# Kernel optimization log

Hardware: AMD Instinct MI355X
Metric: run time of the kernel (lower is better)

The kernel has to match this reference:

```python
import jax, jax.numpy as jnp
import numpy as np

B, N, K, F, L, H, ZMAX = 16, 1024, 16, 128, 4, 128, 100


def setup_inputs() -> dict:
    key = jax.random.key(0)
    ks = jax.random.split(key, 12)
    cell = jnp.eye(3, dtype=jnp.float32)[None] * 8.0 + 0.05 * jax.random.normal(ks[0], (B, 3, 3), dtype=jnp.float32)
    x = jax.random.uniform(ks[1], (B, N, 3), dtype=jnp.float32)
    z = jax.random.randint(ks[2], (B, N), 0, ZMAX)
    struct_size = jnp.full((B,), N, dtype=jnp.int32)
    emb = 0.02 * jax.random.normal(ks[3], (ZMAX, F), dtype=jnp.float32)
    din = 2 * F + 1
    W1 = jax.random.normal(ks[4], (L, din, F), dtype=jnp.float32) / np.sqrt(din)
    b1 = jnp.zeros((L, F), dtype=jnp.float32)
    W2 = jax.random.normal(ks[5], (L, F, F), dtype=jnp.float32) / np.sqrt(F)
    b2 = jnp.zeros((L, F), dtype=jnp.float32)
    A1 = jax.random.normal(ks[6], (din, H), dtype=jnp.float32) / np.sqrt(din)
    a1 = jnp.zeros((H,), dtype=jnp.float32)
    A2 = jax.random.normal(ks[7], (H, 1), dtype=jnp.float32) / np.sqrt(H)
    a2 = jnp.zeros((1,), dtype=jnp.float32)
    return {"cell": cell, "x": x, "z": z, "struct_size": struct_size, "emb": emb,
            "W1": W1, "b1": b1, "W2": W2, "b2": b2, "A1": A1, "a1": a1, "A2": A2, "a2": a2}


def _periodic_knn(cell, frac, k):
    # frac: [B,N,3] fractional coords, cell: [B,3,3] lattice rows.
    b, n, _ = frac.shape
    g = jnp.arange(-1, 2, dtype=frac.dtype)
    shifts = jnp.stack(jnp.meshgrid(g, g, g, indexing="ij"), -1).reshape(-1, 3)  # [27,3]
    rel = frac[:, None, :, :] - frac[:, :, None, :]  # rel[b,i,j] = frac_j - frac_i, [B,N,N,3]

    def body(carry, si):
        bd2, bsi = carry
        s, i = si
        cart = jnp.einsum("bijd,bde->bije", rel + s, cell)
        d2 = jnp.sum(cart * cart, axis=-1)
        upd = d2 < bd2
        return (jnp.where(upd, d2, bd2), jnp.where(upd, i, bsi)), None

    init = (jnp.full((b, n, n), 1e30, dtype=frac.dtype), jnp.zeros((b, n, n), dtype=jnp.int32))
    (d2min, simin), _ = jax.lax.scan(body, init, (shifts, jnp.arange(27, dtype=jnp.int32)))
    eye = jnp.eye(n, dtype=bool)
    d2min = jnp.where(eye[None], 1e30, d2min)  # exclude self (zero-shift) edges
    _, idx = jax.lax.top_k(-d2min, k)  # [B,N,k] neighbor indices
    sid = jnp.take_along_axis(simin, idx, axis=2)  # best image shift per edge
    svec = shifts[sid]  # [B,N,k,3]
    frac_j = jax.vmap(lambda f, i: f[i])(frac, idx)  # [B,N,k,3]
    vec = jnp.einsum("bnkd,bde->bnke", frac_j - frac[:, :, None, :] + svec, cell)
    d = jnp.sqrt(jnp.maximum(jnp.sum(vec * vec, axis=-1), 1e-12))  # [B,N,k]
    return idx, vec, d


def _edge_feat(h, idx, d):
    hj = jax.vmap(lambda hb, ib: hb[ib])(h, idx)  # [B,N,k,F]
    hi = jnp.broadcast_to(h[:, :, None, :], hj.shape)
    return jnp.concatenate([hi, hj, d[..., None]], axis=-1)  # [B,N,k,2F+1]


def reference(cell, x, z, struct_size, emb, W1, b1, W2, b2, A1, a1, A2, a2):
    frac = jnp.mod(x, 1.0)
    idx, vec, d = _periodic_knn(cell, frac, K)
    h = emb[z]  # [B,N,F]
    for l in range(W1.shape[0]):
        feat = _edge_feat(h, idx, d)
        m = jax.nn.silu(feat @ W1[l] + b1[l]) @ W2[l] + b2[l]  # [B,N,k,F]
        h = h + jnp.mean(m, axis=2)
    feat = _edge_feat(h, idx, d)
    w = jax.nn.silu(feat @ A1 + a1) @ A2 + a2  # [B,N,k,1]
    delta_cart = jnp.sum(w * vec, axis=2)  # [B,N,3]
    delta_frac = jnp.einsum("bnd,bde->bne", delta_cart, jnp.linalg.inv(cell))
    return x + delta_frac
```

## Files before the change

### kernel.cpp

```cpp
#include <hip/hip_runtime.h>

#define B_ 16
#define N_ 1024
#define K_ 16
#define F_ 128
#define L_ 4
#define DIN_ 257

typedef __bf16 bf16x8 __attribute__((ext_vector_type(8)));
typedef float f32x4 __attribute__((ext_vector_type(4)));

__device__ __forceinline__ float silu_f(float x) {
    return x / (1.0f + __expf(-x));
}

__device__ __forceinline__ unsigned short f2bf_bits(float f) {
    unsigned u = __builtin_bit_cast(unsigned, f);
    return (unsigned short)((u + 0x7FFFu + ((u >> 16) & 1u)) >> 16);
}

__global__ __launch_bounds__(256) void k_prep(const int* __restrict__ z,
                                              const float* __restrict__ emb,
                                              const float* __restrict__ W1,
                                              const float* __restrict__ W2,
                                              const float* __restrict__ A1,
                                              float* __restrict__ h,
                                              unsigned short* __restrict__ hbf,
                                              unsigned short* __restrict__ Wt1,
                                              unsigned short* __restrict__ Wt2,
                                              unsigned short* __restrict__ At1) {
    int gid = blockIdx.x * 256 + threadIdx.x;
    int id = gid;
    if (id < L_ * 256 * 128) {
        int k = id & 127, n = (id >> 7) & 255, l = id >> 15;
        float v = (n < 128) ? W1[(size_t)l * DIN_ * F_ + (size_t)k * F_ + n]
                            : W1[(size_t)l * DIN_ * F_ + (size_t)(128 + k) * F_ + (n - 128)];
        Wt1[id] = f2bf_bits(v);
    } else {
        int id2 = id - L_ * 256 * 128;
        if (id2 < L_ * 128 * 128) {
            int k = id2 & 127, n = (id2 >> 7) & 127, l = id2 >> 14;
            Wt2[id2] = f2bf_bits(W2[(size_t)l * F_ * F_ + (size_t)k * F_ + n]);
        } else {
            int id3 = id2 - L_ * 128 * 128;
            if (id3 < 256 * 128) {
                int k = id3 & 127, n = id3 >> 7;
                float v = (n < 128) ? A1[(size_t)k * 128 + n]
                                    : A1[(size_t)(128 + k) * 128 + (n - 128)];
                At1[id3] = f2bf_bits(v);
            }
        }
    }
    {
        int t = gid;
        int node = t >> 5;
        int f4 = (t & 31) << 2;
        int zi = z[node];
        float4 v = *reinterpret_cast<const float4*>(&emb[zi * F_ + f4]);
        *reinterpret_cast<float4*>(&h[node * F_ + f4]) = v;
        ushort4 pk;
        pk.x = f2bf_bits(v.x); pk.y = f2bf_bits(v.y);
        pk.z = f2bf_bits(v.z); pk.w = f2bf_bits(v.w);
        *reinterpret_cast<ushort4*>(&hbf[node * F_ + f4]) = pk;
    }
}

__global__ __launch_bounds__(256) void k_front(const float* __restrict__ x,
                                               const float* __restrict__ cell,
                                               int* __restrict__ idx_o,
                                               float* __restrict__ vec_o,
                                               float* __restrict__ d_o,
                                               const unsigned short* __restrict__ hbf,
                                               const unsigned short* __restrict__ Wt1,
                                               float* __restrict__ uv0) {
    __shared__ float fr[N_ * 3];
    int gb = blockIdx.x;
    int wave = threadIdx.x >> 6;
    int lane = threadIdx.x & 63;

    if (gb < 1024) {
        int tile = gb * 4 + wave;
        int mt = tile >> 3, nt = tile & 7;
        int fr16 = lane & 15, ko = lane >> 4;
        const unsigned short* Ap = hbf + (size_t)(mt * 32 + fr16) * 128 + ko * 8;
        const unsigned short* Bp = Wt1 + (size_t)(nt * 32 + fr16) * 128 + ko * 8;
        f32x4 acc00 = {0.f, 0.f, 0.f, 0.f}, acc01 = acc00, acc10 = acc00, acc11 = acc00;
#pragma unroll
        for (int ks = 0; ks < 4; ++ks) {
            bf16x8 a0 = *reinterpret_cast<const bf16x8*>(Ap + ks * 32);
            bf16x8 a1 = *reinterpret_cast<const bf16x8*>(Ap + 16 * 128 + ks * 32);
            bf16x8 b0 = *reinterpret_cast<const bf16x8*>(Bp + ks * 32);
            bf16x8 b1 = *reinterpret_cast<const bf16x8*>(Bp + 16 * 128 + ks * 32);
            acc00 = __builtin_amdgcn_mfma_f32_16x16x32_bf16(a0, b0, acc00, 0, 0, 0);
            acc01 = __builtin_amdgcn_mfma_f32_16x16x32_bf16(a0, b1, acc01, 0, 0, 0);
            acc10 = __builtin_amdgcn_mfma_f32_16x16x32_bf16(a1, b0, acc10, 0, 0, 0);
            acc11 = __builtin_amdgcn_mfma_f32_16x16x32_bf16(a1, b1, acc11, 0, 0, 0);
        }
        int mrow = mt * 32 + ko * 4;
        int cbase = nt * 32 + fr16;
#define EPI_(FM, FN, ACC)                                                    \
    {                                                                        \
        int cc = cbase + FN * 16;                                            \
        _Pragma("unroll") for (int r = 0; r < 4; ++r) {                      \
            int row = mrow + FM * 16 + r;                                    \
            uv0[(size_t)row * 256 + cc] = ACC[r];                            \
        }                                                                    \
    }
        EPI_(0, 0, acc00) EPI_(0, 1, acc01) EPI_(1, 0, acc10) EPI_(1, 1, acc11)
#undef EPI_
        return;
    }

    int kb = gb - 1024;
    int b = kb >> 8;
    int ib = (kb & 255) << 2;
    const float* xb = x + b * N_ * 3;
    for (int u = threadIdx.x; u < N_ * 3; u += 256) {
        float xv = xb[u];
        fr[u] = xv - floorf(xv);
    }
    __syncthreads();
    int i = ib + wave;

    const float* cb = cell + b * 9;
    float c00 = cb[0], c01 = cb[1], c02 = cb[2];
    float c10 = cb[3], c11 = cb[4], c12 = cb[5];
    float c20 = cb[6], c21 = cb[7], c22 = cb[8];
    float fi0 = fr[i * 3 + 0], fi1 = fr[i * 3 + 1], fi2 = fr[i * 3 + 2];

    unsigned long long k[16];
#pragma unroll
    for (int t = 0; t < 16; ++t) {
        int j = t * 64 + lane;
        float r0 = fr[j * 3 + 0] - fi0;
        float r1 = fr[j * 3 + 1] - fi1;
        float r2 = fr[j * 3 + 2] - fi2;
        float s0f = (r0 > 0.f) ? -1.f : 0.f;
        float s1f = (r1 > 0.f) ? -1.f : 0.f;
        float s2f = (r2 > 0.f) ? -1.f : 0.f;
        int sid_base = ((r0 > 0.f) ? 0 : 9) + ((r1 > 0.f) ? 0 : 3) + ((r2 > 0.f) ? 0 : 1);
        float rx0 = r0 + s0f, rx1 = r0 + (s0f + 1.0f);
        float ry0 = r1 + s1f, ry1 = r1 + (s1f + 1.0f);
        float rz0 = r2 + s2f, rz1 = r2 + (s2f + 1.0f);
        float best = 3e38f;
        int bsid = 0;
#pragma unroll
        for (int cbo = 0; cbo < 8; ++cbo) {
            float rs0 = (cbo & 4) ? rx1 : rx0;
            float rs1 = (cbo & 2) ? ry1 : ry0;
            float rs2 = (cbo & 1) ? rz1 : rz0;
            float cx = fmaf(rs2, c20, fmaf(rs1, c10, rs0 * c00));
            float cy = fmaf(rs2, c21, fmaf(rs1, c11, rs0 * c01));
            float cz = fmaf(rs2, c22, fmaf(rs1, c12, rs0 * c02));
            float d2 = fmaf(cz, cz, fmaf(cy, cy, cx * cx));
            int sid = sid_base + ((cbo >> 2) & 1) * 9 + ((cbo >> 1) & 1) * 3 + (cbo & 1);
            if (d2 < best) { best = d2; bsid = sid; }
        }
        if (j == i) best = 3e38f;
        unsigned db = __builtin_bit_cast(unsigned, best);
        k[t] = ((unsigned long long)db << 32) | (unsigned)((j << 5) | bsid);
    }

#define CE_(a, b)                                              \
    {                                                          \
        unsigned long long x_ = k[a], y_ = k[b];               \
        bool s_ = y_ < x_;                                     \
        k[a] = s_ ? y_ : x_;                                   \
        k[b] = s_ ? x_ : y_;                                   \
    }
    CE_(0,1) CE_(2,3) CE_(4,5) CE_(6,7) CE_(8,9) CE_(10,11) CE_(12,13) CE_(14,15)
    CE_(0,2) CE_(1,3) CE_(4,6) CE_(5,7) CE_(8,10) CE_(9,11) CE_(12,14) CE_(13,15)
    CE_(1,2) CE_(5,6) CE_(9,10) CE_(13,14)
    CE_(0,4) CE_(1,5) CE_(2,6) CE_(3,7) CE_(8,12) CE_(9,13) CE_(10,14) CE_(11,15)
    CE_(2,4) CE_(3,5) CE_(10,12) CE_(11,13)
    CE_(1,2) CE_(3,4) CE_(5,6) CE_(9,10) CE_(11,12) CE_(13,14)
    CE_(0,8) CE_(1,9) CE_(2,10) CE_(3,11) CE_(4,12) CE_(5,13) CE_(6,14) CE_(7,15)
    CE_(4,8) CE_(5,9) CE_(6,10) CE_(7,11)
    CE_(2,4) CE_(3,5) CE_(6,8) CE_(7,9) CE_(10,12) CE_(11,13)
    CE_(1,2) CE_(3,4) CE_(5,6) CE_(7,8) CE_(9,10) CE_(11,12) CE_(13,14)
#undef CE_

    unsigned long long sel = 0;
    for (int r = 0; r < 16; ++r) {
        unsigned long long m = k[0];
#pragma unroll
        for (int off = 32; off >= 1; off >>= 1) {
            unsigned long long o = __shfl_xor(m, off);
            if (o < m) m = o;
        }
        if (k[0] == m) {
#pragma unroll
            for (int t = 0; t < 15; ++t) k[t] = k[t + 1];
            k[15] = ~0ull;
        }
        if (lane == r) sel = m;
    }

    if (lane < 16) {
        unsigned pk = (unsigned)sel;
        int j = pk >> 5, sid = pk & 31;
        int s0 = sid / 9 - 1, s1 = (sid / 3) % 3 - 1, s2 = sid % 3 - 1;
        float rs0 = (fr[j * 3 + 0] - fi0) + (float)s0;
        float rs1 = (fr[j * 3 + 1] - fi1) + (float)s1;
        float rs2 = (fr[j * 3 + 2] - fi2) + (float)s2;
        float vx = fmaf(rs2, c20, fmaf(rs1, c10, rs0 * c00));
        float vy = fmaf(rs2, c21, fmaf(rs1, c11, rs0 * c01));
        float vz = fmaf(rs2, c22, fmaf(rs1, c12, rs0 * c02));
        float d2 = fmaf(vz, vz, fmaf(vy, vy, vx * vx));
        float dd = sqrtf(fmaxf(d2, 1e-12f));
        int node = b * N_ + i;
        int eo = node * K_ + lane;
        idx_o[eo] = j;
        d_o[eo] = dd;
        vec_o[eo * 3 + 0] = vx;
        vec_o[eo * 3 + 1] = vy;
        vec_o[eo * 3 + 2] = vz;
    }
}

__global__ __launch_bounds__(256) void k_layer16(const float* __restrict__ UVin,
                                                 const int* __restrict__ idx,
                                                 const float* __restrict__ nd,
                                                 const float* __restrict__ w1d,
                                                 const float* __restrict__ b1l,
                                                 const unsigned short* __restrict__ W2t,
                                                 const float* __restrict__ b2l,
                                                 float* __restrict__ h,
                                                 const unsigned short* __restrict__ W1n,
                                                 float* __restrict__ UVout) {
    __shared__ unsigned short svl[16][136];
    __shared__ unsigned short hbl[16][136];
    int tid = threadIdx.x;
    int gb = blockIdx.x;
    int batch = (gb & 7) + 8 * (gb >> 9);
    int ib = (gb >> 3) & 63;
    int node0 = batch * N_ + ib * 16;
    int bbase = batch * N_;
    int wave = tid >> 6, lane = tid & 63;
    int fr16 = lane & 15, ko = lane >> 4;

    {
        int gn = tid >> 4, fc = tid & 15, f0 = fc << 3;
        int node = node0 + gn;
        int4 ji[4];
        float4 di[4];
#pragma unroll
        for (int q = 0; q < 4; ++q) {
            ji[q] = *reinterpret_cast<const int4*>(&idx[node * K_ + q * 4]);
            di[q] = *reinterpret_cast<const float4*>(&nd[node * K_ + q * 4]);
        }
        float u[8], wd[8], bb[8], acc[8];
#pragma unroll
        for (int q = 0; q < 8; q += 4) {
            float4 t = *reinterpret_cast<const float4*>(&UVin[(size_t)node * 256 + f0 + q]);
            u[q] = t.x; u[q + 1] = t.y; u[q + 2] = t.z; u[q + 3] = t.w;
            float4 t2 = *reinterpret_cast<const float4*>(&w1d[f0 + q]);
            wd[q] = t2.x; wd[q + 1] = t2.y; wd[q + 2] = t2.z; wd[q + 3] = t2.w;
            float4 t3 = *reinterpret_cast<const float4*>(&b1l[f0 + q]);
            bb[q] = t3.x; bb[q + 1] = t3.y; bb[q + 2] = t3.z; bb[q + 3] = t3.w;
        }
#pragma unroll
        for (int q = 0; q < 8; ++q) acc[q] = 0.f;
#pragma unroll
        for (int eq = 0; eq < 4; ++eq) {
            int j4[4] = {ji[eq].x, ji[eq].y, ji[eq].z, ji[eq].w};
            float d4[4] = {di[eq].x, di[eq].y, di[eq].z, di[eq].w};
            float4 va[4], vb[4];
#pragma unroll
            for (int e = 0; e < 4; ++e) {
                const float* vp = &UVin[(size_t)(bbase + j4[e]) * 256 + 128 + f0];
                va[e] = *reinterpret_cast<const float4*>(&vp[0]);
                vb[e] = *reinterpret_cast<const float4*>(&vp[4]);
            }
#pragma unroll
            for (int e = 0; e < 4; ++e) {
                float dd = d4[e];
                float v8[8] = {va[e].x, va[e].y, va[e].z, va[e].w,
                               vb[e].x, vb[e].y, vb[e].z, vb[e].w};
#pragma unroll
                for (int w = 0; w < 8; ++w) {
                    float pre = u[w] + v8[w] + fmaf(dd, wd[w], bb[w]);
                    acc[w] += silu_f(pre);
                }
            }
        }
        const float inv_k = 1.0f / (float)K_;
        unsigned ow[4];
#pragma unroll
        for (int q = 0; q < 4; ++q)
            ow[q] = (unsigned)f2bf_bits(acc[2 * q] * inv_k) |
                    ((unsigned)f2bf_bits(acc[2 * q + 1] * inv_k) << 16);
        *reinterpret_cast<int4*>(&svl[gn][f0]) = make_int4(ow[0], ow[1], ow[2], ow[3]);
    }
    __syncthreads();

    {
        const unsigned short* Bp = W2t + (size_t)(wave * 32 + fr16) * 128 + ko * 8;
        bf16x8 a0[4], b0[4], b1f[4];
#pragma unroll
        for (int ks = 0; ks < 4; ++ks) {
            a0[ks] = *reinterpret_cast<const bf16x8*>(&svl[fr16][ks * 32 + ko * 8]);
            b0[ks] = *reinterpret_cast<const bf16x8*>(Bp + ks * 32);
            b1f[ks] = *reinterpret_cast<const bf16x8*>(Bp + 16 * 128 + ks * 32);
        }
        f32x4 acc00 = {0.f, 0.f, 0.f, 0.f}, acc01 = acc00;
#pragma unroll
        for (int ks = 0; ks < 4; ++ks) {
            acc00 = __builtin_amdgcn_mfma_f32_16x16x32_bf16(a0[ks], b0[ks], acc00, 0, 0, 0);
            acc01 = __builtin_amdgcn_mfma_f32_16x16x32_bf16(a0[ks], b1f[ks], acc01, 0, 0, 0);
        }
        int cb0 = wave * 32 + fr16;
#define EPI2_(FN, ACC)                                                         \
    {                                                                          \
        int col = cb0 + FN * 16;                                               \
        float bv = b2l[col];                                                   \
        _Pragma("unroll") for (int r = 0; r < 4; ++r) {                        \
            int row = ko * 4 + r;                                              \
            int grow = node0 + row;                                            \
            float val = ACC[r] + bv + h[(size_t)grow * 128 + col];             \
            h[(size_t)grow * 128 + col] = val;                                 \
            hbl[row][col] = f2bf_bits(val);                                    \
        }                                                                      \
    }
        EPI2_(0, acc00) EPI2_(1, acc01)
#undef EPI2_
    }
    __syncthreads();

#pragma unroll
    for (int half = 0; half < 2; ++half) {
        int nt2 = wave + half * 4;
        const unsigned short* Bp = W1n + (size_t)(nt2 * 32 + fr16) * 128 + ko * 8;
        bf16x8 a0[4], b0[4], b1f[4];
#pragma unroll
        for (int ks = 0; ks < 4; ++ks) {
            a0[ks] = *reinterpret_cast<const bf16x8*>(&hbl[fr16][ks * 32 + ko * 8]);
            b0[ks] = *reinterpret_cast<const bf16x8*>(Bp + ks * 32);
            b1f[ks] = *reinterpret_cast<const bf16x8*>(Bp + 16 * 128 + ks * 32);
        }
        f32x4 acc00 = {0.f, 0.f, 0.f, 0.f}, acc01 = acc00;
#pragma unroll
        for (int ks = 0; ks < 4; ++ks) {
            acc00 = __builtin_amdgcn_mfma_f32_16x16x32_bf16(a0[ks], b0[ks], acc00, 0, 0, 0);
            acc01 = __builtin_amdgcn_mfma_f32_16x16x32_bf16(a0[ks], b1f[ks], acc01, 0, 0, 0);
        }
        int cb0 = nt2 * 32 + fr16;
#define EPI1_(FN, ACC)                                                         \
    {                                                                          \
        int col = cb0 + FN * 16;                                               \
        _Pragma("unroll") for (int r = 0; r < 4; ++r) {                        \
            int row = ko * 4 + r;                                              \
            UVout[(size_t)(node0 + row) * 256 + col] = ACC[r];                 \
        }                                                                      \
    }
        EPI1_(0, acc00) EPI1_(1, acc01)
#undef EPI1_
    }
}

__global__ __launch_bounds__(256) void k_final(const float* __restrict__ P,
                                               const int* __restrict__ idx,
                                               const float* __restrict__ nd,
                                               const float* __restrict__ nvec,
                                               const float* __restrict__ A1d,
                                               const float* __restrict__ a1v,
                                               const float* __restrict__ A2v,
                                               const float* __restrict__ a2v,
                                               const float* __restrict__ x,
                                               const float* __restrict__ cell,
                                               float* __restrict__ out) {
    __shared__ float plds[16][256];
    __shared__ float wlds[16][17];
    __shared__ float dclds[16][3];
    int gb = blockIdx.x;
    int batch = (gb & 7) + 8 * (gb >> 9);
    int ib = (gb >> 3) & 63;
    int node0 = batch * N_ + ib * 16;
    int bbase = batch * N_;
    int g = threadIdx.x >> 4, fc = threadIdx.x & 15;
    int node = node0 + g;
    int f0 = fc * 8;
    int4 ji[4];
    float4 di[4];
#pragma unroll
    for (int q = 0; q < 4; ++q) {
        ji[q] = *reinterpret_cast<const int4*>(&idx[node * K_ + q * 4]);
        di[q] = *reinterpret_cast<const float4*>(&nd[node * K_ + q * 4]);
    }
    float pa[8], ad[8], aa[8], a2r[8];
#pragma unroll
    for (int q = 0; q < 8; q += 4) {
        float4 t = *reinterpret_cast<const float4*>(&P[(size_t)node * 256 + f0 + q]);
        pa[q] = t.x; pa[q + 1] = t.y; pa[q + 2] = t.z; pa[q + 3] = t.w;
        float4 t2 = *reinterpret_cast<const float4*>(&A1d[f0 + q]);
        ad[q] = t2.x; ad[q + 1] = t2.y; ad[q + 2] = t2.z; ad[q + 3] = t2.w;
        float4 t3 = *reinterpret_cast<const float4*>(&a1v[f0 + q]);
        aa[q] = t3.x; aa[q + 1] = t3.y; aa[q + 2] = t3.z; aa[q + 3] = t3.w;
        float4 t4 = *reinterpret_cast<const float4*>(&A2v[f0 + q]);
        a2r[q] = t4.x; a2r[q + 1] = t4.y; a2r[q + 2] = t4.z; a2r[q + 3] = t4.w;
    }
#pragma unroll
    for (int eq = 0; eq < 4; ++eq) {
        int j4[4] = {ji[eq].x, ji[eq].y, ji[eq].z, ji[eq].w};
        float d4[4] = {di[eq].x, di[eq].y, di[eq].z, di[eq].w};
        float4 va[4], vb[4];
#pragma unroll
        for (int e = 0; e < 4; ++e) {
            const float* vp = &P[(size_t)(bbase + j4[e]) * 256 + 128 + f0];
            va[e] = *reinterpret_cast<const float4*>(&vp[0]);
            vb[e] = *reinterpret_cast<const float4*>(&vp[4]);
        }
#pragma unroll
        for (int e = 0; e < 4; ++e) {
            float dd = d4[e];
            float v8[8] = {va[e].x, va[e].y, va[e].z, va[e].w,
                           vb[e].x, vb[e].y, vb[e].z, vb[e].w};
            float part = 0.f;
#pragma unroll
            for (int w = 0; w < 8; ++w) {
                float pre = pa[w] + v8[w] + fmaf(dd, ad[w], aa[w]);
                part = fmaf(silu_f(pre), a2r[w], part);
            }
            plds[eq * 4 + e][(g << 4) | fc] = part;
        }
    }
    __syncthreads();
    {
        int g2 = threadIdx.x >> 4, e2 = threadIdx.x & 15;
        float w = a2v[0];
#pragma unroll
        for (int f2 = 0; f2 < 16; ++f2) w += plds[e2][(g2 << 4) | f2];
        wlds[g2][e2] = w;
    }
    __syncthreads();
    if (threadIdx.x < 48) {
        int gg = threadIdx.x & 15, c = threadIdx.x >> 4;
        int noded = node0 + gg;
        float dc = 0.f;
#pragma unroll
        for (int e = 0; e < K_; ++e)
            dc = fmaf(wlds[gg][e], nvec[(size_t)(noded * K_ + e) * 3 + c], dc);
        dclds[gg][c] = dc;
    }
    __syncthreads();
    if (threadIdx.x < 48) {
        int gg = threadIdx.x & 15, c = threadIdx.x >> 4;
        int noded = node0 + gg;
        const float* cb = cell + batch * 9;
        float c00 = cb[0], c01 = cb[1], c02 = cb[2];
        float c10 = cb[3], c11 = cb[4], c12 = cb[5];
        float c20 = cb[6], c21 = cb[7], c22 = cb[8];
        float det = c00 * (c11 * c22 - c12 * c21) - c01 * (c10 * c22 - c12 * c20) +
                    c02 * (c10 * c21 - c11 * c20);
        float rdet = 1.0f / det;
        float i0c, i1c, i2c;
        if (c == 0) {
            i0c = (c11 * c22 - c12 * c21) * rdet;
            i1c = -(c10 * c22 - c12 * c20) * rdet;
            i2c = (c10 * c21 - c11 * c20) * rdet;
        } else if (c == 1) {
            i0c = -(c01 * c22 - c02 * c21) * rdet;
            i1c = (c00 * c22 - c02 * c20) * rdet;
            i2c = -(c00 * c21 - c01 * c20) * rdet;
        } else {
            i0c = (c01 * c12 - c02 * c11) * rdet;
            i1c = -(c00 * c12 - c02 * c10) * rdet;
            i2c = (c00 * c11 - c01 * c10) * rdet;
        }
        float df = dclds[gg][0] * i0c + dclds[gg][1] * i1c + dclds[gg][2] * i2c;
        out[(size_t)noded * 3 + c] = x[(size_t)noded * 3 + c] + df;
    }
}

extern "C" void kernel_launch(void* const* d_in, const int* in_sizes, int n_in,
                              void* d_out, int out_size, void* d_ws, size_t ws_size,
                              hipStream_t stream) {
    (void)in_sizes; (void)n_in; (void)out_size; (void)ws_size;
    const float* cell = (const float*)d_in[0];
    const float* x    = (const float*)d_in[1];
    const int*   z    = (const int*)d_in[2];
    const float* emb  = (const float*)d_in[4];
    const float* W1   = (const float*)d_in[5];
    const float* b1   = (const float*)d_in[6];
    const float* W2   = (const float*)d_in[7];
    const float* b2   = (const float*)d_in[8];
    const float* A1   = (const float*)d_in[9];
    const float* a1   = (const float*)d_in[10];
    const float* A2   = (const float*)d_in[11];
    const float* a2   = (const float*)d_in[12];
    float* out = (float*)d_out;

    char* ws = (char*)d_ws;
    size_t off = 0;
    auto alloc = [&](size_t bytes) {
        void* p = ws + off;
        off = (off + bytes + 255) & ~(size_t)255;
        return p;
    };
    int* idx    = (int*)alloc((size_t)B_ * N_ * K_ * 4);
    float* nd   = (float*)alloc((size_t)B_ * N_ * K_ * 4);
    float* nvec = (float*)alloc((size_t)B_ * N_ * K_ * 3 * 4);
    float* h0   = (float*)alloc((size_t)B_ * N_ * F_ * 4);
    float* uv0  = (float*)alloc((size_t)B_ * N_ * 256 * 4);
    float* uv1  = (float*)alloc((size_t)B_ * N_ * 256 * 4);
    unsigned short* hbf = (unsigned short*)alloc((size_t)B_ * N_ * F_ * 2);
    unsigned short* Wt1 = (unsigned short*)alloc((size_t)L_ * 256 * 128 * 2);
    unsigned short* Wt2 = (unsigned short*)alloc((size_t)L_ * 128 * 128 * 2);
    unsigned short* At1 = (unsigned short*)alloc((size_t)256 * 128 * 2);

    k_prep<<<2048, 256, 0, stream>>>(z, emb, W1, W2, A1, h0, hbf, Wt1, Wt2, At1);
    k_front<<<5120, 256, 0, stream>>>(x, cell, idx, nvec, nd, hbf, Wt1, uv0);

    for (int l = 0; l < L_; ++l) {
        const float* uin = (l & 1) ? uv1 : uv0;
        float* uout = (l & 1) ? uv0 : uv1;
        const unsigned short* W1next = (l < 3) ? (Wt1 + (size_t)(l + 1) * 256 * 128) : At1;
        k_layer16<<<1024, 256, 0, stream>>>(uin, idx, nd,
                                            W1 + (size_t)l * DIN_ * F_ + 256 * F_,
                                            b1 + l * F_, Wt2 + (size_t)l * 128 * 128,
                                            b2 + l * F_, h0, W1next, uout);
    }
    k_final<<<1024, 256, 0, stream>>>(uv0, idx, nd, nvec, A1 + 256 * F_, a1, A2, a2, x, cell,
                                      out);
}
```

Before: 268.0 us.

## Halve nodes per block in layer kernel and split neighbor loop across thread halves

The layer kernel now handles 8 nodes per block instead of 16, and the launch grid doubles to 2048 blocks. The two halves of the block each process 8 of the 16 neighbors and combine their partial sums through shared memory. The MFMA tiles are still 16 rows, so the unused rows are zero-padded and the epilogue writes only the valid half. The goal is more parallelism and shorter per-thread gather chains, at the cost of half-wasted MFMA work, reloading weights in twice as many blocks, and an extra barrier.

```diff
diff --git a/kernel.cpp b/kernel.cpp
--- a/kernel.cpp
+++ b/kernel.cpp
@@ -218,36 +218,46 @@
     }
 }
 
-__global__ __launch_bounds__(256) void k_layer16(const float* __restrict__ UVin,
-                                                 const int* __restrict__ idx,
-                                                 const float* __restrict__ nd,
-                                                 const float* __restrict__ w1d,
-                                                 const float* __restrict__ b1l,
-                                                 const unsigned short* __restrict__ W2t,
-                                                 const float* __restrict__ b2l,
-                                                 float* __restrict__ h,
-                                                 const unsigned short* __restrict__ W1n,
-                                                 float* __restrict__ UVout) {
-    __shared__ unsigned short svl[16][136];
-    __shared__ unsigned short hbl[16][136];
+__global__ __launch_bounds__(256) void k_layer8(const float* __restrict__ UVin,
+                                                const int* __restrict__ idx,
+                                                const float* __restrict__ nd,
+                                                const float* __restrict__ w1d,
+                                                const float* __restrict__ b1l,
+                                                const unsigned short* __restrict__ W2t,
+                                                const float* __restrict__ b2l,
+                                                float* __restrict__ h,
+                                                const unsigned short* __restrict__ W1n,
+                                                float* __restrict__ UVout) {
+    __shared__ __align__(16) unsigned short svl[16][136];
+    __shared__ __align__(16) unsigned short hbl[16][136];
+    __shared__ float partial[8][132];
     int tid = threadIdx.x;
     int gb = blockIdx.x;
-    int batch = (gb & 7) + 8 * (gb >> 9);
-    int ib = (gb >> 3) & 63;
-    int node0 = batch * N_ + ib * 16;
+    int batch = (gb & 7) + 8 * (gb >> 10);
+    int ib = (gb >> 3) & 127;
+    int node0 = batch * N_ + ib * 8;
     int bbase = batch * N_;
     int wave = tid >> 6, lane = tid & 63;
     int fr16 = lane & 15, ko = lane >> 4;
 
+    for (int u = tid; u < 272; u += 256) {
+        if (u < 136)
+            reinterpret_cast<int4*>(&svl[8][0])[u] = make_int4(0, 0, 0, 0);
+        else
+            reinterpret_cast<int4*>(&hbl[8][0])[u - 136] = make_int4(0, 0, 0, 0);
+    }
+
     {
-        int gn = tid >> 4, fc = tid & 15, f0 = fc << 3;
+        int eh = tid >> 7;
+        int tq = tid & 127;
+        int gn = tq >> 4, fc = tq & 15, f0 = fc << 3;
         int node = node0 + gn;
-        int4 ji[4];
-        float4 di[4];
-#pragma unroll
-        for (int q = 0; q < 4; ++q) {
-            ji[q] = *reinterpret_cast<const int4*>(&idx[node * K_ + q * 4]);
-            di[q] = *reinterpret_cast<const float4*>(&nd[node * K_ + q * 4]);
+        int4 ji[2];
+        float4 di[2];
+#pragma unroll
+        for (int q = 0; q < 2; ++q) {
+            ji[q] = *reinterpret_cast<const int4*>(&idx[node * K_ + eh * 8 + q * 4]);
+            di[q] = *reinterpret_cast<const float4*>(&nd[node * K_ + eh * 8 + q * 4]);
         }
         float u[8], wd[8], bb[8], acc[8];
 #pragma unroll
@@ -262,7 +272,7 @@
 #pragma unroll
         for (int q = 0; q < 8; ++q) acc[q] = 0.f;
 #pragma unroll
-        for (int eq = 0; eq < 4; ++eq) {
+        for (int eq = 0; eq < 2; ++eq) {
             int j4[4] = {ji[eq].x, ji[eq].y, ji[eq].z, ji[eq].w};
             float d4[4] = {di[eq].x, di[eq].y, di[eq].z, di[eq].w};
             float4 va[4], vb[4];
@@ -284,13 +294,22 @@
                 }
             }
         }
-        const float inv_k = 1.0f / (float)K_;
-        unsigned ow[4];
-#pragma unroll
-        for (int q = 0; q < 4; ++q)
-            ow[q] = (unsigned)f2bf_bits(acc[2 * q] * inv_k) |
-                    ((unsigned)f2bf_bits(acc[2 * q + 1] * inv_k) << 16);
-        *reinterpret_cast<int4*>(&svl[gn][f0]) = make_int4(ow[0], ow[1], ow[2], ow[3]);
+        if (eh == 1) {
+#pragma unroll
+            for (int q = 0; q < 8; ++q) partial[gn][f0 + q] = acc[q];
+        }
+        __syncthreads();
+        if (eh == 0) {
+            const float inv_k = 1.0f / (float)K_;
+            unsigned ow[4];
+#pragma unroll
+            for (int q = 0; q < 8; ++q) acc[q] += partial[gn][f0 + q];
+#pragma unroll
+            for (int q = 0; q < 4; ++q)
+                ow[q] = (unsigned)f2bf_bits(acc[2 * q] * inv_k) |
+                        ((unsigned)f2bf_bits(acc[2 * q + 1] * inv_k) << 16);
+            *reinterpret_cast<int4*>(&svl[gn][f0]) = make_int4(ow[0], ow[1], ow[2], ow[3]);
+        }
     }
     __syncthreads();
 
@@ -310,6 +329,7 @@
             acc01 = __builtin_amdgcn_mfma_f32_16x16x32_bf16(a0[ks], b1f[ks], acc01, 0, 0, 0);
         }
         int cb0 = wave * 32 + fr16;
+        if (ko < 2) {
 #define EPI2_(FN, ACC)                                                         \
     {                                                                          \
         int col = cb0 + FN * 16;                                               \
@@ -322,8 +342,9 @@
             hbl[row][col] = f2bf_bits(val);                                    \
         }                                                                      \
     }
-        EPI2_(0, acc00) EPI2_(1, acc01)
+            EPI2_(0, acc00) EPI2_(1, acc01)
 #undef EPI2_
+        }
     }
     __syncthreads();
 
@@ -345,6 +366,7 @@
             acc01 = __builtin_amdgcn_mfma_f32_16x16x32_bf16(a0[ks], b1f[ks], acc01, 0, 0, 0);
         }
         int cb0 = nt2 * 32 + fr16;
+        if (ko < 2) {
 #define EPI1_(FN, ACC)                                                         \
     {                                                                          \
         int col = cb0 + FN * 16;                                               \
@@ -353,8 +375,9 @@
             UVout[(size_t)(node0 + row) * 256 + col] = ACC[r];                 \
         }                                                                      \
     }
-        EPI1_(0, acc00) EPI1_(1, acc01)
+            EPI1_(0, acc00) EPI1_(1, acc01)
 #undef EPI1_
+        }
     }
 }
 
@@ -515,10 +538,10 @@
         const float* uin = (l & 1) ? uv1 : uv0;
         float* uout = (l & 1) ? uv0 : uv1;
         const unsigned short* W1next = (l < 3) ? (Wt1 + (size_t)(l + 1) * 256 * 128) : At1;
-        k_layer16<<<1024, 256, 0, stream>>>(uin, idx, nd,
-                                            W1 + (size_t)l * DIN_ * F_ + 256 * F_,
-                                            b1 + l * F_, Wt2 + (size_t)l * 128 * 128,
-                                            b2 + l * F_, h0, W1next, uout);
+        k_layer8<<<2048, 256, 0, stream>>>(uin, idx, nd,
+                                           W1 + (size_t)l * DIN_ * F_ + 256 * F_,
+                                           b1 + l * F_, Wt2 + (size_t)l * 128 * 128,
+                                           b2 + l * F_, h0, W1next, uout);
     }
     k_final<<<1024, 256, 0, stream>>>(uv0, idx, nd, nvec, A1 + 256 * F_, a1, A2, a2, x, cell,
                                       out);
```

Measured after the change: 285.6 us. +6.6%, slower.
